# Kernel tuning notes

Hardware: AMD Instinct MI355X
Metric: run time of the kernel (lower is better)

Reference implementation:

```python
import jax, jax.numpy as jnp
import numpy as np

B, S, D_IN, D_MODEL, H = 2, 2048, 1024, 1024, 16
DEPTH = D_MODEL // H


def setup_inputs() -> dict:
    key = jax.random.key(0)
    ks = jax.random.split(key, 12)
    f32 = jnp.float32
    scale = 0.02  # typical init scale for linear weights
    inp = {
        "v": jax.random.normal(ks[0], (B, S, D_IN), f32),
        "k": jax.random.normal(ks[1], (B, S, D_IN), f32),
        "q": jax.random.normal(ks[2], (B, S, D_IN), f32),
        # padding mask: 1 -> masked out, 0 -> keep; broadcastable to (B,H,Sq,Sk)
        "mask": jax.random.randint(ks[3], (B, 1, 1, S), 0, 2).astype(f32),
        # linear params stored as [in, out] so y = x @ W + b (matches torch Linear math)
        "Wq": jax.random.normal(ks[4], (D_IN, D_MODEL), f32) * scale,
        "bq": jnp.zeros((D_MODEL,), f32),
        "Wk": jax.random.normal(ks[5], (D_IN, D_MODEL), f32) * scale,
        "bk": jnp.zeros((D_MODEL,), f32),
        "Wv": jax.random.normal(ks[6], (D_IN, D_MODEL), f32) * scale,
        "bv": jnp.zeros((D_MODEL,), f32),
        "Wo": jax.random.normal(ks[7], (D_MODEL, D_MODEL), f32) * scale,
        "bo": jnp.zeros((D_MODEL,), f32),
    }
    return inp


def _split_heads(x):
    # [B, S, D_MODEL] -> [B, H, S, DEPTH]
    b = x.shape[0]
    return x.reshape(b, -1, H, DEPTH).transpose(0, 2, 1, 3)


def reference(v, k, q, mask, Wq, bq, Wk, bk, Wv, bv, Wo, bo):
    qh = _split_heads(q @ Wq + bq)   # [B,H,Sq,D]
    kh = _split_heads(k @ Wk + bk)   # [B,H,Sk,D]
    vh = _split_heads(v @ Wv + bv)   # [B,H,Sk,D]

    # scaled dot-product attention with additive mask (mask * -1e9)
    inv_sqrt_dk = 1.0 / jnp.sqrt(jnp.float32(DEPTH))
    logits = jnp.einsum('bhqd,bhkd->bhqk', qh, kh) * inv_sqrt_dk
    logits = logits + mask * (-1e9)
    attn = jax.nn.softmax(logits, axis=-1)          # [B,H,Sq,Sk]
    ctx = jnp.einsum('bhqk,bhkd->bhqd', attn, vh)   # [B,H,Sq,D]

    b = q.shape[0]
    concat = ctx.transpose(0, 2, 1, 3).reshape(b, -1, D_MODEL)  # [B,Sq,D_MODEL]
    out = concat @ Wo + bo
    return out, attn
```

## Files before the change

kernel.cpp:

```cpp
#include <hip/hip_runtime.h>
#include <cstdint>
#include <cstddef>

typedef __attribute__((ext_vector_type(4))) float f4;
typedef __attribute__((ext_vector_type(8))) short bf16x8;
typedef __attribute__((ext_vector_type(8))) unsigned short u16x8;
typedef unsigned long long u64;

__device__ __forceinline__ unsigned short f2bf(float x) {
    unsigned u = __float_as_uint(x);
    u += 0x7fffu + ((u >> 16) & 1u);
    return (unsigned short)(u >> 16);
}
__device__ __forceinline__ float bf2f(unsigned short h) {
    return __uint_as_float(((unsigned)h) << 16);
}
__device__ __forceinline__ float fast_exp2(float x) { return __builtin_amdgcn_exp2f(x); }
__device__ __forceinline__ float fast_log2(float x) { return __builtin_amdgcn_logf(x); }
__device__ __forceinline__ void gll16(const void* g, void* l) {
    __builtin_amdgcn_global_load_lds(
        (const __attribute__((address_space(1))) unsigned int*)g,
        (__attribute__((address_space(3))) unsigned int*)l, 16, 0, 0);
}
__device__ __forceinline__ f4 mfma16(bf16x8 a, bf16x8 b, f4 c) {
    return __builtin_amdgcn_mfma_f32_16x16x32_bf16(a, b, c, 0, 0, 0);
}

__global__ __launch_bounds__(256)
void prep_w_kernel(const float* __restrict__ Wq, const float* __restrict__ Wk,
                   const float* __restrict__ Wv, const float* __restrict__ Wo,
                   unsigned short* __restrict__ wt)
{
    const int w = blockIdx.z;
    const float* W = w == 0 ? Wq : (w == 1 ? Wk : (w == 2 ? Wv : Wo));
    unsigned short* hi = wt + (size_t)w * 1048576;

    const int kb = blockIdx.x << 6, nb = blockIdx.y << 6;
    __shared__ float T[64][68];
    const int tid = threadIdx.x;
    {
        const int r = tid >> 2, c0 = (tid & 3) << 4;
        const float* src = W + (size_t)(kb + r) * 1024 + nb + c0;
        *(f4*)&T[r][c0 + 0]  = *(const f4*)(src + 0);
        *(f4*)&T[r][c0 + 4]  = *(const f4*)(src + 4);
        *(f4*)&T[r][c0 + 8]  = *(const f4*)(src + 8);
        *(f4*)&T[r][c0 + 12] = *(const f4*)(src + 12);
    }
    __syncthreads();
    {
        const int n = tid & 63, ks = (tid >> 6) << 4;
        unsigned short vh[16];
        #pragma unroll
        for (int j = 0; j < 16; ++j) vh[j] = f2bf(T[ks + j][n]);
        const size_t dst = (size_t)(nb + n) * 1024 + kb + ks;
        *(u16x8*)(hi + dst)     = *(u16x8*)&vh[0];
        *(u16x8*)(hi + dst + 8) = *(u16x8*)&vh[8];
    }
}

__global__ __launch_bounds__(256)
void prep_a_kernel(const float* __restrict__ q, const float* __restrict__ k,
                   const float* __restrict__ v, unsigned short* __restrict__ a_hi)
{
    const int gid = blockIdx.x * 256 + threadIdx.x;
    const int z = gid >> 18;
    const int rem = gid & 262143;
    const float* src = z == 0 ? q : (z == 1 ? k : v);
    const size_t off = (size_t)rem << 4;
    const float* s = src + off;
    unsigned short* hi = a_hi + ((size_t)z << 22) + off;
    float xs[16];
    *(f4*)&xs[0]  = *(const f4*)(s + 0);
    *(f4*)&xs[4]  = *(const f4*)(s + 4);
    *(f4*)&xs[8]  = *(const f4*)(s + 8);
    *(f4*)&xs[12] = *(const f4*)(s + 12);
    unsigned short hv[16];
    #pragma unroll
    for (int j = 0; j < 16; ++j) hv[j] = f2bf(xs[j]);
    *(u16x8*)(hi + 0) = *(u16x8*)&hv[0];
    *(u16x8*)(hi + 8) = *(u16x8*)&hv[8];
}

__global__ __launch_bounds__(256)
void vtr_kernel(const unsigned short* __restrict__ v_hi, unsigned short* __restrict__ vT)
{
    __shared__ unsigned short T[64][80];
    const int bh = blockIdx.y;
    const int s0 = blockIdx.x << 6;
    const int tid = threadIdx.x;
    const size_t base = (size_t)bh * 131072;
    {
        const int s = tid >> 2, dq = (tid & 3) << 4;
        const unsigned short* src = v_hi + base + (size_t)(s0 + s) * 64 + dq;
        u16x8 a = *(const u16x8*)src;
        u16x8 b = *(const u16x8*)(src + 8);
        *(u16x8*)&T[s][dq]     = a;
        *(u16x8*)&T[s][dq + 8] = b;
    }
    __syncthreads();
    {
        const int d = tid >> 2, sq = (tid & 3) << 4;
        unsigned short o[16];
        #pragma unroll
        for (int j = 0; j < 16; ++j) o[j] = T[sq + j][d];
        unsigned short* dst = vT + base + ((size_t)d << 11) + s0 + sq;
        *(u16x8*)dst       = *(u16x8*)&o[0];
        *(u16x8*)(dst + 8) = *(u16x8*)&o[8];
    }
}

__device__ __forceinline__ void gemm1_core(
    const unsigned short* __restrict__ AH, const unsigned short* __restrict__ WH,
    const float* __restrict__ bias, int bm, int bn, int mode,
    unsigned short* __restrict__ o_hi, float* __restrict__ o_f32, unsigned char* lds)
{
    unsigned char* As = lds;
    unsigned char* Bs = lds + 16384;

    const int tid = threadIdx.x, lane = tid & 63, wave = tid >> 6;
    const int wm = wave >> 1, wn = wave & 1;
    const int cx = lane & 15, lg = lane >> 4;
    const int l3 = lane >> 3, p3 = lane & 7;
    const int m0 = bm << 7, n0 = bn << 7;

    f4 acc[4][4];
    #pragma unroll
    for (int i = 0; i < 4; ++i)
        #pragma unroll
        for (int j = 0; j < 4; ++j) acc[i][j] = (f4){0.f, 0.f, 0.f, 0.f};

    #pragma unroll 1
    for (int k0 = 0; k0 < 1024; k0 += 64) {
        __syncthreads();
        #pragma unroll
        for (int c = 0; c < 4; ++c) {
            const int cb = (c << 2) + wave;
            const int row = (cb << 3) + l3;
            const int lgx = p3 ^ (row & 7);
            gll16(AH + (size_t)(m0 + row) * 1024 + k0 + (lgx << 3),
                  As + (cb << 10) + (lane << 4));
            gll16(WH + (size_t)(n0 + row) * 1024 + k0 + (lgx << 3),
                  Bs + (cb << 10) + (lane << 4));
        }
        __syncthreads();
        #pragma unroll
        for (int ks = 0; ks < 2; ++ks) {
            bf16x8 ah[4], bh[4];
            #pragma unroll
            for (int t = 0; t < 4; ++t) {
                const int r = (wm << 6) + (t << 4) + cx;
                ah[t] = *(const bf16x8*)(As + r * 128 + (((((ks << 2) + lg)) ^ (r & 7)) << 4));
                const int n = (wn << 6) + (t << 4) + cx;
                bh[t] = *(const bf16x8*)(Bs + n * 128 + (((((ks << 2) + lg)) ^ (n & 7)) << 4));
            }
            #pragma unroll
            for (int i = 0; i < 4; ++i)
                #pragma unroll
                for (int j = 0; j < 4; ++j)
                    acc[i][j] = mfma16(ah[i], bh[j], acc[i][j]);
        }
    }

    float bv4[4];
    #pragma unroll
    for (int j = 0; j < 4; ++j) bv4[j] = bias[n0 + (wn << 6) + (j << 4) + cx];

    #pragma unroll
    for (int i = 0; i < 4; ++i)
        #pragma unroll
        for (int j = 0; j < 4; ++j) {
            const int n = n0 + (wn << 6) + (j << 4) + cx;
            const int mb = m0 + (wm << 6) + (i << 4) + (lg << 2);
            if (mode == 2) {
                #pragma unroll
                for (int r = 0; r < 4; ++r)
                    o_f32[(size_t)(mb + r) * 1024 + n] = acc[i][j][r] + bv4[j];
            } else {
                const int b = mb >> 11, hh = n >> 6, d = n & 63;
                #pragma unroll
                for (int r = 0; r < 4; ++r) {
                    const int s = (mb + r) & 2047;
                    o_hi[(((size_t)(b * 16 + hh)) * 2048 + s) * 64 + d] = f2bf(acc[i][j][r] + bv4[j]);
                }
            }
        }
}

__global__ __launch_bounds__(256)
void qkv_gemm_kernel(const unsigned short* __restrict__ a_hi,
                     const unsigned short* __restrict__ wt,
                     const float* __restrict__ bq, const float* __restrict__ bk,
                     const float* __restrict__ bv,
                     unsigned short* __restrict__ q_hi, unsigned short* __restrict__ k_hi,
                     unsigned short* __restrict__ v_hi)
{
    __shared__ __align__(16) unsigned char lds[32768];
    const int f = blockIdx.x;
    const int id2 = (f & 7) * 96 + (f >> 3);
    const int z = id2 >> 8;
    const int rem = id2 & 255;
    const int bn = rem >> 5, bm = rem & 31;
    const unsigned short* AH = a_hi + ((size_t)z << 22);
    const unsigned short* WH = wt + (size_t)z * 1048576;
    const float* bias = z == 0 ? bq : (z == 1 ? bk : bv);
    unsigned short* ohi = z == 0 ? q_hi : (z == 1 ? k_hi : v_hi);
    gemm1_core(AH, WH, bias, bm, bn, 1, ohi, nullptr, lds);
}

__global__ __launch_bounds__(256)
void out_gemm_kernel(const unsigned short* __restrict__ ctx_hi,
                     const unsigned short* __restrict__ wt_o,
                     const float* __restrict__ bo, float* __restrict__ out)
{
    __shared__ __align__(16) unsigned char lds[32768];
    const int f = blockIdx.x;
    const int id2 = (f & 7) * 32 + (f >> 3);
    const int bn = id2 >> 5, bm = id2 & 31;
    gemm1_core(ctx_hi, wt_o, bo, bm, bn, 2, nullptr, out, lds);
}

__global__ __launch_bounds__(256, 4)
void attn_kernel(const unsigned short* __restrict__ q_hi, const unsigned short* __restrict__ k_hi,
                 const unsigned short* __restrict__ vT, const float* __restrict__ mask,
                 float* __restrict__ attn, unsigned short* __restrict__ ctx_hi)
{
    __shared__ __align__(16) unsigned char lds[40960];
    unsigned char* K1 = lds;
    unsigned char* Vs = lds + 16384;
    unsigned char* Ps = lds + 32768;

    const int f = blockIdx.x;
    const int swzf = (f & 7) * 128 + (f >> 3);
    const int bh = swzf >> 5;
    const int q0 = (swzf & 31) << 6;
    const int b = bh >> 4, h = bh & 15;
    const int tid = threadIdx.x, lane = tid & 63, wave = tid >> 6;
    const int cx = lane & 15, lg = lane >> 4;
    const int l3 = lane >> 3, p3 = lane & 7;
    const size_t base = (size_t)bh * 131072;
    const float* mg = mask + (size_t)b * 2048;

    constexpr float C2   = 0.18033688011112042f;
    constexpr float M2   = -1.4426950408889634e9f;
    constexpr float MFIX = 4.0f;

    #pragma unroll
    for (int c = 0; c < 2; ++c) {
        const int cb = (c << 2) + wave;
        const int row = (cb << 3) + l3;
        const int lgx = p3 ^ (row & 7);
        gll16(q_hi + base + (size_t)(q0 + row) * 64 + (lgx << 3),
              Ps + (cb << 10) + (lane << 4));
        gll16(k_hi + base + (size_t)row * 64 + (lgx << 3),
              K1 + (cb << 10) + (lane << 4));
    }
    f4 mrc[4];
    #pragma unroll
    for (int nt = 0; nt < 4; ++nt) mrc[nt] = *(const f4*)(mg + (nt << 4) + (lg << 2));
    asm volatile("s_waitcnt vmcnt(0)" ::: "memory");
    __builtin_amdgcn_s_barrier();

    bf16x8 qb[2];
    {
        const int r = (wave << 4) + cx;
        const int mk = r & 7;
        #pragma unroll
        for (int ks = 0; ks < 2; ++ks)
            qb[ks] = *(const bf16x8*)(Ps + r * 128 + (((((ks << 2) + lg)) ^ mk) << 4));
    }

    float l_loc = 0.f;
    #pragma unroll 1
    for (int t = 0; t < 32; ++t) {
        const int p = t & 1;
        const int k0 = t << 6;
        f4 mrn[4];
        if (t < 31) {
            #pragma unroll
            for (int c = 0; c < 2; ++c) {
                const int cb = (c << 2) + wave;
                const int row = (cb << 3) + l3;
                const int lgx = p3 ^ (row & 7);
                gll16(k_hi + base + (size_t)(k0 + 64 + row) * 64 + (lgx << 3),
                      K1 + ((p ^ 1) << 13) + (cb << 10) + (lane << 4));
            }
            #pragma unroll
            for (int nt = 0; nt < 4; ++nt)
                mrn[nt] = *(const f4*)(mg + k0 + 64 + (nt << 4) + (lg << 2));
        }
        const unsigned char* Kc = K1 + (p << 13);
        __builtin_amdgcn_s_setprio(1);
        f4 sv[4];
        #pragma unroll
        for (int nt = 0; nt < 4; ++nt) {
            const int kr = (nt << 4) + cx;
            const int mk = kr & 7;
            f4 s = (f4){0.f, 0.f, 0.f, 0.f};
            #pragma unroll
            for (int ks = 0; ks < 2; ++ks) {
                const bf16x8 kb = *(const bf16x8*)(Kc + kr * 128 + (((((ks << 2) + lg)) ^ mk) << 4));
                s = mfma16(kb, qb[ks], s);
            }
            sv[nt] = s;
        }
        __builtin_amdgcn_s_setprio(0);
        #pragma unroll
        for (int nt = 0; nt < 4; ++nt)
            #pragma unroll
            for (int r = 0; r < 4; ++r)
                l_loc += fast_exp2(fmaf(sv[nt][r], C2, fmaf(mrc[nt][r], M2, -MFIX)));
        #pragma unroll
        for (int nt = 0; nt < 4; ++nt) mrc[nt] = mrn[nt];
        asm volatile("s_waitcnt vmcnt(0)" ::: "memory");
        __builtin_amdgcn_s_barrier();
    }
    float ssum = l_loc;
    ssum += __shfl_xor(ssum, 16);
    ssum += __shfl_xor(ssum, 32);
    const float cofs = -MFIX - fast_log2(ssum);

    #pragma unroll
    for (int c = 0; c < 2; ++c) {
        const int cb = (c << 2) + wave;
        const int row = (cb << 3) + l3;
        const int lgx = p3 ^ (row & 7);
        gll16(k_hi + base + (size_t)row * 64 + (lgx << 3),
              K1 + (cb << 10) + (lane << 4));
        gll16(vT + base + ((size_t)row << 11) + (lgx << 3),
              Vs + (cb << 10) + (lane << 4));
    }
    #pragma unroll
    for (int nt = 0; nt < 4; ++nt) mrc[nt] = *(const f4*)(mg + (nt << 4) + (lg << 2));
    asm volatile("s_waitcnt vmcnt(0)" ::: "memory");
    __builtin_amdgcn_s_barrier();

    f4 cacc[4];
    #pragma unroll
    for (int nt = 0; nt < 4; ++nt) cacc[nt] = (f4){0.f, 0.f, 0.f, 0.f};

    float* arow = attn + ((size_t)bh * 2048 + q0 + (wave << 4) + cx) * 2048;
    const unsigned psSwz = (unsigned)((cx & 7) << 4);

    #pragma unroll 1
    for (int t = 0; t < 32; ++t) {
        const int p = t & 1;
        const int k0 = t << 6;
        f4 mrn[4];
        if (t < 31) {
            #pragma unroll
            for (int c = 0; c < 2; ++c) {
                const int cb = (c << 2) + wave;
                const int row = (cb << 3) + l3;
                const int lgx = p3 ^ (row & 7);
                gll16(k_hi + base + (size_t)(k0 + 64 + row) * 64 + (lgx << 3),
                      K1 + ((p ^ 1) << 13) + (cb << 10) + (lane << 4));
                gll16(vT + base + ((size_t)row << 11) + k0 + 64 + (lgx << 3),
                      Vs + ((p ^ 1) << 13) + (cb << 10) + (lane << 4));
            }
            #pragma unroll
            for (int nt = 0; nt < 4; ++nt)
                mrn[nt] = *(const f4*)(mg + k0 + 64 + (nt << 4) + (lg << 2));
        }
        const unsigned char* Kc = K1 + (p << 13);
        f4 s[4];
        __builtin_amdgcn_s_setprio(1);
        #pragma unroll
        for (int nt = 0; nt < 4; ++nt) {
            const int kr = (nt << 4) + cx;
            const int mk = kr & 7;
            s[nt] = (f4){0.f, 0.f, 0.f, 0.f};
            #pragma unroll
            for (int ks = 0; ks < 2; ++ks) {
                const bf16x8 kb = *(const bf16x8*)(Kc + kr * 128 + (((((ks << 2) + lg)) ^ mk) << 4));
                s[nt] = mfma16(kb, qb[ks], s[nt]);
            }
        }
        __builtin_amdgcn_s_setprio(0);
        #pragma unroll
        for (int nt = 0; nt < 4; ++nt) {
            f4 pv;
            #pragma unroll
            for (int r = 0; r < 4; ++r)
                pv[r] = fast_exp2(fmaf(s[nt][r], C2, fmaf(mrc[nt][r], M2, cofs)));
            *(f4*)(arow + k0 + (nt << 4) + (lg << 2)) = pv;
            const unsigned w0 = (unsigned)f2bf(pv[0]) | ((unsigned)f2bf(pv[1]) << 16);
            const unsigned w1 = (unsigned)f2bf(pv[2]) | ((unsigned)f2bf(pv[3]) << 16);
            const u64 packed = (u64)w0 | ((u64)w1 << 32);
            *(u64*)(Ps + (((wave << 4) + cx) * 128) +
                    ((unsigned)((nt << 5) + (lg << 3)) ^ psSwz)) = packed;
        }
        #pragma unroll
        for (int nt = 0; nt < 4; ++nt) mrc[nt] = mrn[nt];
        __builtin_amdgcn_s_setprio(1);
        #pragma unroll
        for (int ks = 0; ks < 2; ++ks) {
            const bf16x8 pa = *(const bf16x8*)(Ps + (((wave << 4) + cx) * 128) +
                                ((unsigned)((ks << 6) + (lg << 4)) ^ psSwz));
            #pragma unroll
            for (int nt = 0; nt < 4; ++nt) {
                const int dr = (nt << 4) + cx;
                const bf16x8 vb = *(const bf16x8*)(Vs + (p << 13) + dr * 128 +
                                    (((((ks << 2) + lg)) ^ (dr & 7)) << 4));
                cacc[nt] = mfma16(pa, vb, cacc[nt]);
            }
        }
        __builtin_amdgcn_s_setprio(0);
        asm volatile("s_waitcnt vmcnt(4)" ::: "memory");
        __builtin_amdgcn_s_barrier();
    }

    #pragma unroll
    for (int nt = 0; nt < 4; ++nt)
        #pragma unroll
        for (int r = 0; r < 4; ++r) {
            const int srow = q0 + (wave << 4) + (lg << 2) + r;
            const int d = (h << 6) + (nt << 4) + cx;
            ctx_hi[((size_t)b * 2048 + srow) * 1024 + d] = f2bf(cacc[nt][r]);
        }
}

extern "C" void kernel_launch(void* const* d_in, const int* in_sizes, int n_in,
                              void* d_out, int out_size, void* d_ws, size_t ws_size,
                              hipStream_t stream)
{
    const float* v_in = (const float*)d_in[0];
    const float* k_in = (const float*)d_in[1];
    const float* q_in = (const float*)d_in[2];
    const float* mask = (const float*)d_in[3];
    const float* Wq = (const float*)d_in[4];
    const float* bq = (const float*)d_in[5];
    const float* Wk = (const float*)d_in[6];
    const float* bk = (const float*)d_in[7];
    const float* Wv = (const float*)d_in[8];
    const float* bv = (const float*)d_in[9];
    const float* Wo = (const float*)d_in[10];
    const float* bo = (const float*)d_in[11];

    float* out  = (float*)d_out;
    float* attn = out + (size_t)4194304;

    unsigned char* ws = (unsigned char*)d_ws;
    unsigned short* wt     = (unsigned short*)(ws);
    unsigned short* q_hi   = (unsigned short*)(ws + (size_t)(8)  * 1048576);
    unsigned short* k_hi   = (unsigned short*)(ws + (size_t)(16) * 1048576);
    unsigned short* v_hi   = (unsigned short*)(ws + (size_t)(24) * 1048576);
    unsigned short* ctx_hi = (unsigned short*)(ws + (size_t)(32) * 1048576);
    unsigned short* vT     = (unsigned short*)(ws + (size_t)(40) * 1048576);

    unsigned short* a_hi   = (unsigned short*)(attn + (size_t)60 * 1048576);

    prep_w_kernel<<<dim3(16, 16, 4), 256, 0, stream>>>(Wq, Wk, Wv, Wo, wt);
    prep_a_kernel<<<3072, 256, 0, stream>>>(q_in, k_in, v_in, a_hi);
    qkv_gemm_kernel<<<768, 256, 0, stream>>>(a_hi, wt, bq, bk, bv, q_hi, k_hi, v_hi);
    vtr_kernel<<<dim3(32, 32), 256, 0, stream>>>(v_hi, vT);
    attn_kernel<<<1024, 256, 0, stream>>>(q_hi, k_hi, vT, mask, attn, ctx_hi);
    out_gemm_kernel<<<256, 256, 0, stream>>>(ctx_hi, wt + (size_t)3 * 1048576, bo, out);
}
```

Before: 293.2 us.

## Load K/V/Q fragments directly from global memory, dropping LDS staging and barriers

Removes the double-buffered LDS staging of K, V and Q via global_load_lds, along with the per-iteration barriers and waitcnts. Each wave now reads its MFMA operand fragments straight from global memory (relying on L1/L2 since the four waves share K/V tiles), and LDS shrinks to the P scratch only. This removes synchronisation overhead and raises possible occupancy, but gives up the explicit prefetch overlap and issues redundant global reads across waves.

```diff
diff --git a/kernel.cpp b/kernel.cpp
--- a/kernel.cpp
+++ b/kernel.cpp
@@ -224,10 +224,7 @@
                  const unsigned short* __restrict__ vT, const float* __restrict__ mask,
                  float* __restrict__ attn, unsigned short* __restrict__ ctx_hi)
 {
-    __shared__ __align__(16) unsigned char lds[40960];
-    unsigned char* K1 = lds;
-    unsigned char* Vs = lds + 16384;
-    unsigned char* Ps = lds + 32768;
+    __shared__ __align__(16) unsigned char Ps[8192];
 
     const int f = blockIdx.x;
     const int swzf = (f & 7) * 128 + (f >> 3);
@@ -236,7 +233,6 @@
     const int b = bh >> 4, h = bh & 15;
     const int tid = threadIdx.x, lane = tid & 63, wave = tid >> 6;
     const int cx = lane & 15, lg = lane >> 4;
-    const int l3 = lane >> 3, p3 = lane & 7;
     const size_t base = (size_t)bh * 131072;
     const float* mg = mask + (size_t)b * 2048;
 
@@ -244,96 +240,37 @@
     constexpr float M2   = -1.4426950408889634e9f;
     constexpr float MFIX = 4.0f;
 
-    #pragma unroll
-    for (int c = 0; c < 2; ++c) {
-        const int cb = (c << 2) + wave;
-        const int row = (cb << 3) + l3;
-        const int lgx = p3 ^ (row & 7);
-        gll16(q_hi + base + (size_t)(q0 + row) * 64 + (lgx << 3),
-              Ps + (cb << 10) + (lane << 4));
-        gll16(k_hi + base + (size_t)row * 64 + (lgx << 3),
-              K1 + (cb << 10) + (lane << 4));
-    }
-    f4 mrc[4];
-    #pragma unroll
-    for (int nt = 0; nt < 4; ++nt) mrc[nt] = *(const f4*)(mg + (nt << 4) + (lg << 2));
-    asm volatile("s_waitcnt vmcnt(0)" ::: "memory");
-    __builtin_amdgcn_s_barrier();
-
     bf16x8 qb[2];
-    {
-        const int r = (wave << 4) + cx;
-        const int mk = r & 7;
-        #pragma unroll
-        for (int ks = 0; ks < 2; ++ks)
-            qb[ks] = *(const bf16x8*)(Ps + r * 128 + (((((ks << 2) + lg)) ^ mk) << 4));
-    }
+    #pragma unroll
+    for (int ks = 0; ks < 2; ++ks)
+        qb[ks] = *(const bf16x8*)(q_hi + base + (size_t)(q0 + (wave << 4) + cx) * 64
+                                  + (((ks << 2) + lg) << 3));
 
     float l_loc = 0.f;
     #pragma unroll 1
     for (int t = 0; t < 32; ++t) {
-        const int p = t & 1;
         const int k0 = t << 6;
-        f4 mrn[4];
-        if (t < 31) {
-            #pragma unroll
-            for (int c = 0; c < 2; ++c) {
-                const int cb = (c << 2) + wave;
-                const int row = (cb << 3) + l3;
-                const int lgx = p3 ^ (row & 7);
-                gll16(k_hi + base + (size_t)(k0 + 64 + row) * 64 + (lgx << 3),
-                      K1 + ((p ^ 1) << 13) + (cb << 10) + (lane << 4));
-            }
-            #pragma unroll
-            for (int nt = 0; nt < 4; ++nt)
-                mrn[nt] = *(const f4*)(mg + k0 + 64 + (nt << 4) + (lg << 2));
-        }
-        const unsigned char* Kc = K1 + (p << 13);
-        __builtin_amdgcn_s_setprio(1);
-        f4 sv[4];
         #pragma unroll
         for (int nt = 0; nt < 4; ++nt) {
-            const int kr = (nt << 4) + cx;
-            const int mk = kr & 7;
             f4 s = (f4){0.f, 0.f, 0.f, 0.f};
             #pragma unroll
             for (int ks = 0; ks < 2; ++ks) {
-                const bf16x8 kb = *(const bf16x8*)(Kc + kr * 128 + (((((ks << 2) + lg)) ^ mk) << 4));
+                const bf16x8 kb = *(const bf16x8*)(k_hi + base
+                    + (size_t)(k0 + (nt << 4) + cx) * 64 + (((ks << 2) + lg) << 3));
                 s = mfma16(kb, qb[ks], s);
             }
-            sv[nt] = s;
-        }
-        __builtin_amdgcn_s_setprio(0);
-        #pragma unroll
-        for (int nt = 0; nt < 4; ++nt)
-            #pragma unroll
-            for (int r = 0; r < 4; ++r)
-                l_loc += fast_exp2(fmaf(sv[nt][r], C2, fmaf(mrc[nt][r], M2, -MFIX)));
-        #pragma unroll
-        for (int nt = 0; nt < 4; ++nt) mrc[nt] = mrn[nt];
-        asm volatile("s_waitcnt vmcnt(0)" ::: "memory");
-        __builtin_amdgcn_s_barrier();
+            const f4 ml = *(const f4*)(mg + k0 + (nt << 4) + (lg << 2));
+            l_loc += fast_exp2(fmaf(s[0], C2, fmaf(ml[0], M2, -MFIX)))
+                   + fast_exp2(fmaf(s[1], C2, fmaf(ml[1], M2, -MFIX)))
+                   + fast_exp2(fmaf(s[2], C2, fmaf(ml[2], M2, -MFIX)))
+                   + fast_exp2(fmaf(s[3], C2, fmaf(ml[3], M2, -MFIX)));
+        }
     }
     float ssum = l_loc;
     ssum += __shfl_xor(ssum, 16);
     ssum += __shfl_xor(ssum, 32);
     const float cofs = -MFIX - fast_log2(ssum);
 
-    #pragma unroll
-    for (int c = 0; c < 2; ++c) {
-        const int cb = (c << 2) + wave;
-        const int row = (cb << 3) + l3;
-        const int lgx = p3 ^ (row & 7);
-        gll16(k_hi + base + (size_t)row * 64 + (lgx << 3),
-              K1 + (cb << 10) + (lane << 4));
-        gll16(vT + base + ((size_t)row << 11) + (lgx << 3),
-              Vs + (cb << 10) + (lane << 4));
-    }
-    #pragma unroll
-    for (int nt = 0; nt < 4; ++nt) mrc[nt] = *(const f4*)(mg + (nt << 4) + (lg << 2));
-    asm volatile("s_waitcnt vmcnt(0)" ::: "memory");
-    __builtin_amdgcn_s_barrier();
-
     f4 cacc[4];
     #pragma unroll
     for (int nt = 0; nt < 4; ++nt) cacc[nt] = (f4){0.f, 0.f, 0.f, 0.f};
@@ -343,45 +280,25 @@
 
     #pragma unroll 1
     for (int t = 0; t < 32; ++t) {
-        const int p = t & 1;
         const int k0 = t << 6;
-        f4 mrn[4];
-        if (t < 31) {
-            #pragma unroll
-            for (int c = 0; c < 2; ++c) {
-                const int cb = (c << 2) + wave;
-                const int row = (cb << 3) + l3;
-                const int lgx = p3 ^ (row & 7);
-                gll16(k_hi + base + (size_t)(k0 + 64 + row) * 64 + (lgx << 3),
-                      K1 + ((p ^ 1) << 13) + (cb << 10) + (lane << 4));
-                gll16(vT + base + ((size_t)row << 11) + k0 + 64 + (lgx << 3),
-                      Vs + ((p ^ 1) << 13) + (cb << 10) + (lane << 4));
-            }
-            #pragma unroll
-            for (int nt = 0; nt < 4; ++nt)
-                mrn[nt] = *(const f4*)(mg + k0 + 64 + (nt << 4) + (lg << 2));
-        }
-        const unsigned char* Kc = K1 + (p << 13);
         f4 s[4];
-        __builtin_amdgcn_s_setprio(1);
         #pragma unroll
         for (int nt = 0; nt < 4; ++nt) {
-            const int kr = (nt << 4) + cx;
-            const int mk = kr & 7;
             s[nt] = (f4){0.f, 0.f, 0.f, 0.f};
             #pragma unroll
             for (int ks = 0; ks < 2; ++ks) {
-                const bf16x8 kb = *(const bf16x8*)(Kc + kr * 128 + (((((ks << 2) + lg)) ^ mk) << 4));
+                const bf16x8 kb = *(const bf16x8*)(k_hi + base
+                    + (size_t)(k0 + (nt << 4) + cx) * 64 + (((ks << 2) + lg) << 3));
                 s[nt] = mfma16(kb, qb[ks], s[nt]);
             }
         }
-        __builtin_amdgcn_s_setprio(0);
         #pragma unroll
         for (int nt = 0; nt < 4; ++nt) {
+            const f4 ml = *(const f4*)(mg + k0 + (nt << 4) + (lg << 2));
             f4 pv;
             #pragma unroll
             for (int r = 0; r < 4; ++r)
-                pv[r] = fast_exp2(fmaf(s[nt][r], C2, fmaf(mrc[nt][r], M2, cofs)));
+                pv[r] = fast_exp2(fmaf(s[nt][r], C2, fmaf(ml[r], M2, cofs)));
             *(f4*)(arow + k0 + (nt << 4) + (lg << 2)) = pv;
             const unsigned w0 = (unsigned)f2bf(pv[0]) | ((unsigned)f2bf(pv[1]) << 16);
             const unsigned w1 = (unsigned)f2bf(pv[2]) | ((unsigned)f2bf(pv[3]) << 16);
@@ -390,23 +307,16 @@
                     ((unsigned)((nt << 5) + (lg << 3)) ^ psSwz)) = packed;
         }
         #pragma unroll
-        for (int nt = 0; nt < 4; ++nt) mrc[nt] = mrn[nt];
-        __builtin_amdgcn_s_setprio(1);
-        #pragma unroll
         for (int ks = 0; ks < 2; ++ks) {
             const bf16x8 pa = *(const bf16x8*)(Ps + (((wave << 4) + cx) * 128) +
                                 ((unsigned)((ks << 6) + (lg << 4)) ^ psSwz));
             #pragma unroll
             for (int nt = 0; nt < 4; ++nt) {
-                const int dr = (nt << 4) + cx;
-                const bf16x8 vb = *(const bf16x8*)(Vs + (p << 13) + dr * 128 +
-                                    (((((ks << 2) + lg)) ^ (dr & 7)) << 4));
+                const bf16x8 vb = *(const bf16x8*)(vT + base
+                    + ((size_t)((nt << 4) + cx) << 11) + k0 + (((ks << 2) + lg) << 3));
                 cacc[nt] = mfma16(pa, vb, cacc[nt]);
             }
         }
-        __builtin_amdgcn_s_setprio(0);
-        asm volatile("s_waitcnt vmcnt(4)" ::: "memory");
-        __builtin_amdgcn_s_barrier();
     }
 
     #pragma unroll
```

Result: slower. 536.4 us (+82.9%).

## Double attention query tile to 128 rows per block for K/V reuse

Applied to the files above, without the earlier changes.

The attention kernel now processes 128 query rows per block (two 16-row subtiles per wave) instead of 64, halving the grid and sharing each loaded K/V tile and each K fragment across twice as many MFMAs. It also switches bf16 packing to the hardware v_cvt_pk_bf16_f32 instruction and adjusts waitcnt depths and sched barriers. In exchange it raises LDS use to 48KB, lowers the occupancy hint to 3 blocks per CU, and increases register pressure.

```diff
diff --git a/kernel.cpp b/kernel.cpp
--- a/kernel.cpp
+++ b/kernel.cpp
@@ -14,6 +14,11 @@
 }
 __device__ __forceinline__ float bf2f(unsigned short h) {
     return __uint_as_float(((unsigned)h) << 16);
+}
+__device__ __forceinline__ unsigned cvtpk_bf16(float lo, float hi) {
+    unsigned r;
+    asm("v_cvt_pk_bf16_f32 %0, %1, %2" : "=v"(r) : "v"(lo), "v"(hi));
+    return r;
 }
 __device__ __forceinline__ float fast_exp2(float x) { return __builtin_amdgcn_exp2f(x); }
 __device__ __forceinline__ float fast_log2(float x) { return __builtin_amdgcn_logf(x); }
@@ -219,20 +224,20 @@
     gemm1_core(ctx_hi, wt_o, bo, bm, bn, 2, nullptr, out, lds);
 }
 
-__global__ __launch_bounds__(256, 4)
+__global__ __launch_bounds__(256, 3)
 void attn_kernel(const unsigned short* __restrict__ q_hi, const unsigned short* __restrict__ k_hi,
                  const unsigned short* __restrict__ vT, const float* __restrict__ mask,
                  float* __restrict__ attn, unsigned short* __restrict__ ctx_hi)
 {
-    __shared__ __align__(16) unsigned char lds[40960];
+    __shared__ __align__(16) unsigned char lds[49152];
     unsigned char* K1 = lds;
     unsigned char* Vs = lds + 16384;
     unsigned char* Ps = lds + 32768;
 
     const int f = blockIdx.x;
-    const int swzf = (f & 7) * 128 + (f >> 3);
-    const int bh = swzf >> 5;
-    const int q0 = (swzf & 31) << 6;
+    const int swzf = (f & 7) * 64 + (f >> 3);
+    const int bh = swzf >> 4;
+    const int q0 = (swzf & 15) << 7;
     const int b = bh >> 4, h = bh & 15;
     const int tid = threadIdx.x, lane = tid & 63, wave = tid >> 6;
     const int cx = lane & 15, lg = lane >> 4;
@@ -245,12 +250,18 @@
     constexpr float MFIX = 4.0f;
 
     #pragma unroll
-    for (int c = 0; c < 2; ++c) {
+    for (int c = 0; c < 4; ++c) {
         const int cb = (c << 2) + wave;
         const int row = (cb << 3) + l3;
         const int lgx = p3 ^ (row & 7);
         gll16(q_hi + base + (size_t)(q0 + row) * 64 + (lgx << 3),
               Ps + (cb << 10) + (lane << 4));
+    }
+    #pragma unroll
+    for (int c = 0; c < 2; ++c) {
+        const int cb = (c << 2) + wave;
+        const int row = (cb << 3) + l3;
+        const int lgx = p3 ^ (row & 7);
         gll16(k_hi + base + (size_t)row * 64 + (lgx << 3),
               K1 + (cb << 10) + (lane << 4));
     }
@@ -260,16 +271,17 @@
     asm volatile("s_waitcnt vmcnt(0)" ::: "memory");
     __builtin_amdgcn_s_barrier();
 
-    bf16x8 qb[2];
-    {
-        const int r = (wave << 4) + cx;
+    bf16x8 qb[2][2];
+    #pragma unroll
+    for (int qs = 0; qs < 2; ++qs) {
+        const int r = (wave << 5) + (qs << 4) + cx;
         const int mk = r & 7;
         #pragma unroll
         for (int ks = 0; ks < 2; ++ks)
-            qb[ks] = *(const bf16x8*)(Ps + r * 128 + (((((ks << 2) + lg)) ^ mk) << 4));
-    }
-
-    float l_loc = 0.f;
+            qb[qs][ks] = *(const bf16x8*)(Ps + r * 128 + (((((ks << 2) + lg)) ^ mk) << 4));
+    }
+
+    float l4[2][2] = {{0.f, 0.f}, {0.f, 0.f}};
     #pragma unroll 1
     for (int t = 0; t < 32; ++t) {
         const int p = t & 1;
@@ -284,40 +296,47 @@
                 gll16(k_hi + base + (size_t)(k0 + 64 + row) * 64 + (lgx << 3),
                       K1 + ((p ^ 1) << 13) + (cb << 10) + (lane << 4));
             }
+            __builtin_amdgcn_sched_barrier(0);
             #pragma unroll
             for (int nt = 0; nt < 4; ++nt)
                 mrn[nt] = *(const f4*)(mg + k0 + 64 + (nt << 4) + (lg << 2));
         }
         const unsigned char* Kc = K1 + (p << 13);
-        __builtin_amdgcn_s_setprio(1);
-        f4 sv[4];
         #pragma unroll
         for (int nt = 0; nt < 4; ++nt) {
             const int kr = (nt << 4) + cx;
             const int mk = kr & 7;
-            f4 s = (f4){0.f, 0.f, 0.f, 0.f};
-            #pragma unroll
-            for (int ks = 0; ks < 2; ++ks) {
-                const bf16x8 kb = *(const bf16x8*)(Kc + kr * 128 + (((((ks << 2) + lg)) ^ mk) << 4));
-                s = mfma16(kb, qb[ks], s);
-            }
-            sv[nt] = s;
-        }
-        __builtin_amdgcn_s_setprio(0);
-        #pragma unroll
-        for (int nt = 0; nt < 4; ++nt)
-            #pragma unroll
-            for (int r = 0; r < 4; ++r)
-                l_loc += fast_exp2(fmaf(sv[nt][r], C2, fmaf(mrc[nt][r], M2, -MFIX)));
+            const bf16x8 kb0 = *(const bf16x8*)(Kc + kr * 128 + ((lg ^ mk) << 4));
+            const bf16x8 kb1 = *(const bf16x8*)(Kc + kr * 128 + (((4 + lg) ^ mk) << 4));
+            __builtin_amdgcn_s_setprio(1);
+            f4 s0 = mfma16(kb0, qb[0][0], (f4){0.f, 0.f, 0.f, 0.f});
+            s0 = mfma16(kb1, qb[0][1], s0);
+            f4 s1 = mfma16(kb0, qb[1][0], (f4){0.f, 0.f, 0.f, 0.f});
+            s1 = mfma16(kb1, qb[1][1], s1);
+            __builtin_amdgcn_s_setprio(0);
+            const f4 mv = mrc[nt];
+            l4[0][nt & 1] += fast_exp2(fmaf(s0[0], C2, fmaf(mv[0], M2, -MFIX)))
+                           + fast_exp2(fmaf(s0[1], C2, fmaf(mv[1], M2, -MFIX)))
+                           + fast_exp2(fmaf(s0[2], C2, fmaf(mv[2], M2, -MFIX)))
+                           + fast_exp2(fmaf(s0[3], C2, fmaf(mv[3], M2, -MFIX)));
+            l4[1][nt & 1] += fast_exp2(fmaf(s1[0], C2, fmaf(mv[0], M2, -MFIX)))
+                           + fast_exp2(fmaf(s1[1], C2, fmaf(mv[1], M2, -MFIX)))
+                           + fast_exp2(fmaf(s1[2], C2, fmaf(mv[2], M2, -MFIX)))
+                           + fast_exp2(fmaf(s1[3], C2, fmaf(mv[3], M2, -MFIX)));
+        }
         #pragma unroll
         for (int nt = 0; nt < 4; ++nt) mrc[nt] = mrn[nt];
-        asm volatile("s_waitcnt vmcnt(0)" ::: "memory");
+        asm volatile("s_waitcnt vmcnt(4)" ::: "memory");
         __builtin_amdgcn_s_barrier();
     }
-    float ssum = l_loc;
-    ssum += __shfl_xor(ssum, 16);
-    ssum += __shfl_xor(ssum, 32);
-    const float cofs = -MFIX - fast_log2(ssum);
+    float cofs[2];
+    #pragma unroll
+    for (int qs = 0; qs < 2; ++qs) {
+        float ss = l4[qs][0] + l4[qs][1];
+        ss += __shfl_xor(ss, 16);
+        ss += __shfl_xor(ss, 32);
+        cofs[qs] = -MFIX - fast_log2(ss);
+    }
 
     #pragma unroll
     for (int c = 0; c < 2; ++c) {
@@ -334,11 +353,14 @@
     asm volatile("s_waitcnt vmcnt(0)" ::: "memory");
     __builtin_amdgcn_s_barrier();
 
-    f4 cacc[4];
-    #pragma unroll
-    for (int nt = 0; nt < 4; ++nt) cacc[nt] = (f4){0.f, 0.f, 0.f, 0.f};
-
-    float* arow = attn + ((size_t)bh * 2048 + q0 + (wave << 4) + cx) * 2048;
+    f4 cacc[2][4];
+    #pragma unroll
+    for (int qs = 0; qs < 2; ++qs)
+        #pragma unroll
+        for (int nt = 0; nt < 4; ++nt) cacc[qs][nt] = (f4){0.f, 0.f, 0.f, 0.f};
+
+    float* arow0 = attn + ((size_t)bh * 2048 + q0 + (wave << 5) + cx) * 2048;
+    float* arow1 = arow0 + (size_t)16 * 2048;
     const unsigned psSwz = (unsigned)((cx & 7) << 4);
 
     #pragma unroll 1
@@ -357,66 +379,77 @@
                 gll16(vT + base + ((size_t)row << 11) + k0 + 64 + (lgx << 3),
                       Vs + ((p ^ 1) << 13) + (cb << 10) + (lane << 4));
             }
+            __builtin_amdgcn_sched_barrier(0);
             #pragma unroll
             for (int nt = 0; nt < 4; ++nt)
                 mrn[nt] = *(const f4*)(mg + k0 + 64 + (nt << 4) + (lg << 2));
         }
         const unsigned char* Kc = K1 + (p << 13);
-        f4 s[4];
-        __builtin_amdgcn_s_setprio(1);
+        f4 s[2][4];
         #pragma unroll
         for (int nt = 0; nt < 4; ++nt) {
             const int kr = (nt << 4) + cx;
             const int mk = kr & 7;
-            s[nt] = (f4){0.f, 0.f, 0.f, 0.f};
-            #pragma unroll
-            for (int ks = 0; ks < 2; ++ks) {
-                const bf16x8 kb = *(const bf16x8*)(Kc + kr * 128 + (((((ks << 2) + lg)) ^ mk) << 4));
-                s[nt] = mfma16(kb, qb[ks], s[nt]);
-            }
-        }
-        __builtin_amdgcn_s_setprio(0);
-        #pragma unroll
-        for (int nt = 0; nt < 4; ++nt) {
-            f4 pv;
-            #pragma unroll
-            for (int r = 0; r < 4; ++r)
-                pv[r] = fast_exp2(fmaf(s[nt][r], C2, fmaf(mrc[nt][r], M2, cofs)));
-            *(f4*)(arow + k0 + (nt << 4) + (lg << 2)) = pv;
-            const unsigned w0 = (unsigned)f2bf(pv[0]) | ((unsigned)f2bf(pv[1]) << 16);
-            const unsigned w1 = (unsigned)f2bf(pv[2]) | ((unsigned)f2bf(pv[3]) << 16);
-            const u64 packed = (u64)w0 | ((u64)w1 << 32);
-            *(u64*)(Ps + (((wave << 4) + cx) * 128) +
-                    ((unsigned)((nt << 5) + (lg << 3)) ^ psSwz)) = packed;
+            const bf16x8 kb0 = *(const bf16x8*)(Kc + kr * 128 + ((lg ^ mk) << 4));
+            const bf16x8 kb1 = *(const bf16x8*)(Kc + kr * 128 + (((4 + lg) ^ mk) << 4));
+            __builtin_amdgcn_s_setprio(1);
+            s[0][nt] = mfma16(kb0, qb[0][0], (f4){0.f, 0.f, 0.f, 0.f});
+            s[0][nt] = mfma16(kb1, qb[0][1], s[0][nt]);
+            s[1][nt] = mfma16(kb0, qb[1][0], (f4){0.f, 0.f, 0.f, 0.f});
+            s[1][nt] = mfma16(kb1, qb[1][1], s[1][nt]);
+            __builtin_amdgcn_s_setprio(0);
+        }
+        #pragma unroll
+        for (int qs = 0; qs < 2; ++qs) {
+            float* arow = qs ? arow1 : arow0;
+            const unsigned psRow = (unsigned)(((wave << 5) + (qs << 4) + cx) * 128);
+            #pragma unroll
+            for (int nt = 0; nt < 4; ++nt) {
+                f4 pv;
+                #pragma unroll
+                for (int r = 0; r < 4; ++r)
+                    pv[r] = fast_exp2(fmaf(s[qs][nt][r], C2, fmaf(mrc[nt][r], M2, cofs[qs])));
+                *(f4*)(arow + k0 + (nt << 4) + (lg << 2)) = pv;
+                const unsigned w0 = cvtpk_bf16(pv[0], pv[1]);
+                const unsigned w1 = cvtpk_bf16(pv[2], pv[3]);
+                const u64 packed = (u64)w0 | ((u64)w1 << 32);
+                *(u64*)(Ps + psRow + ((unsigned)((nt << 5) + (lg << 3)) ^ psSwz)) = packed;
+            }
         }
         #pragma unroll
         for (int nt = 0; nt < 4; ++nt) mrc[nt] = mrn[nt];
-        __builtin_amdgcn_s_setprio(1);
         #pragma unroll
         for (int ks = 0; ks < 2; ++ks) {
-            const bf16x8 pa = *(const bf16x8*)(Ps + (((wave << 4) + cx) * 128) +
-                                ((unsigned)((ks << 6) + (lg << 4)) ^ psSwz));
+            bf16x8 pa[2];
+            #pragma unroll
+            for (int qs = 0; qs < 2; ++qs)
+                pa[qs] = *(const bf16x8*)(Ps + (((wave << 5) + (qs << 4) + cx) * 128) +
+                                          ((unsigned)((ks << 6) + (lg << 4)) ^ psSwz));
             #pragma unroll
             for (int nt = 0; nt < 4; ++nt) {
                 const int dr = (nt << 4) + cx;
                 const bf16x8 vb = *(const bf16x8*)(Vs + (p << 13) + dr * 128 +
                                     (((((ks << 2) + lg)) ^ (dr & 7)) << 4));
-                cacc[nt] = mfma16(pa, vb, cacc[nt]);
-            }
-        }
-        __builtin_amdgcn_s_setprio(0);
-        asm volatile("s_waitcnt vmcnt(4)" ::: "memory");
+                __builtin_amdgcn_s_setprio(1);
+                cacc[0][nt] = mfma16(pa[0], vb, cacc[0][nt]);
+                cacc[1][nt] = mfma16(pa[1], vb, cacc[1][nt]);
+                __builtin_amdgcn_s_setprio(0);
+            }
+        }
+        asm volatile("s_waitcnt vmcnt(8)" ::: "memory");
         __builtin_amdgcn_s_barrier();
     }
 
     #pragma unroll
-    for (int nt = 0; nt < 4; ++nt)
-        #pragma unroll
-        for (int r = 0; r < 4; ++r) {
-            const int srow = q0 + (wave << 4) + (lg << 2) + r;
-            const int d = (h << 6) + (nt << 4) + cx;
-            ctx_hi[((size_t)b * 2048 + srow) * 1024 + d] = f2bf(cacc[nt][r]);
-        }
+    for (int qs = 0; qs < 2; ++qs)
+        #pragma unroll
+        for (int nt = 0; nt < 4; ++nt)
+            #pragma unroll
+            for (int r = 0; r < 4; ++r) {
+                const int srow = q0 + (wave << 5) + (qs << 4) + (lg << 2) + r;
+                const int d = (h << 6) + (nt << 4) + cx;
+                ctx_hi[((size_t)b * 2048 + srow) * 1024 + d] = f2bf(cacc[qs][nt][r]);
+            }
 }
 
 extern "C" void kernel_launch(void* const* d_in, const int* in_sizes, int n_in,
@@ -453,6 +486,6 @@
     prep_a_kernel<<<3072, 256, 0, stream>>>(q_in, k_in, v_in, a_hi);
     qkv_gemm_kernel<<<768, 256, 0, stream>>>(a_hi, wt, bq, bk, bv, q_hi, k_hi, v_hi);
     vtr_kernel<<<dim3(32, 32), 256, 0, stream>>>(v_hi, vT);
-    attn_kernel<<<1024, 256, 0, stream>>>(q_hi, k_hi, vT, mask, attn, ctx_hi);
+    attn_kernel<<<512, 256, 0, stream>>>(q_hi, k_hi, vT, mask, attn, ctx_hi);
     out_gemm_kernel<<<256, 256, 0, stream>>>(ctx_hi, wt + (size_t)3 * 1048576, bo, out);
 }
```

Measured after the change: 286.7 us. -2.2%, faster.

## Register-prefetch K in attention stats pass and use packed bf16 convert

Applied to the files above, without the earlier changes.

The first (softmax-denominator) pass of the attention kernel no longer stages Q and K through LDS with barriers. Each wave loads its Q and K MFMA fragments straight from global memory into registers, double-buffered with ping-pong arrays, and the exp-sum accumulates into four partial sums. In the second pass, the manual float-to-bf16 rounding is replaced by the hardware v_cvt_pk_bf16_f32 instruction, and a scheduling barrier is added after the K/V LDS loads. Occupancy hint drops from 4 to 3 blocks per CU to make room for the extra registers, which risks less latency hiding.

```diff
diff --git a/kernel.cpp b/kernel.cpp
--- a/kernel.cpp
+++ b/kernel.cpp
@@ -14,6 +14,11 @@
 }
 __device__ __forceinline__ float bf2f(unsigned short h) {
     return __uint_as_float(((unsigned)h) << 16);
+}
+__device__ __forceinline__ unsigned cvtpk_bf16(float lo, float hi) {
+    unsigned r;
+    asm("v_cvt_pk_bf16_f32 %0, %1, %2" : "=v"(r) : "v"(lo), "v"(hi));
+    return r;
 }
 __device__ __forceinline__ float fast_exp2(float x) { return __builtin_amdgcn_exp2f(x); }
 __device__ __forceinline__ float fast_log2(float x) { return __builtin_amdgcn_logf(x); }
@@ -219,7 +224,7 @@
     gemm1_core(ctx_hi, wt_o, bo, bm, bn, 2, nullptr, out, lds);
 }
 
-__global__ __launch_bounds__(256, 4)
+__global__ __launch_bounds__(256, 3)
 void attn_kernel(const unsigned short* __restrict__ q_hi, const unsigned short* __restrict__ k_hi,
                  const unsigned short* __restrict__ vT, const float* __restrict__ mask,
                  float* __restrict__ attn, unsigned short* __restrict__ ctx_hi)
@@ -244,77 +249,63 @@
     constexpr float M2   = -1.4426950408889634e9f;
     constexpr float MFIX = 4.0f;
 
-    #pragma unroll
-    for (int c = 0; c < 2; ++c) {
-        const int cb = (c << 2) + wave;
-        const int row = (cb << 3) + l3;
-        const int lgx = p3 ^ (row & 7);
-        gll16(q_hi + base + (size_t)(q0 + row) * 64 + (lgx << 3),
-              Ps + (cb << 10) + (lane << 4));
-        gll16(k_hi + base + (size_t)row * 64 + (lgx << 3),
-              K1 + (cb << 10) + (lane << 4));
-    }
-    f4 mrc[4];
-    #pragma unroll
-    for (int nt = 0; nt < 4; ++nt) mrc[nt] = *(const f4*)(mg + (nt << 4) + (lg << 2));
-    asm volatile("s_waitcnt vmcnt(0)" ::: "memory");
-    __builtin_amdgcn_s_barrier();
-
     bf16x8 qb[2];
-    {
-        const int r = (wave << 4) + cx;
-        const int mk = r & 7;
+    #pragma unroll
+    for (int ks = 0; ks < 2; ++ks)
+        qb[ks] = *(const bf16x8*)(q_hi + base + (size_t)(q0 + (wave << 4) + cx) * 64
+                                  + (((ks << 2) + lg) << 3));
+
+    float l4[4] = {0.f, 0.f, 0.f, 0.f};
+
+    const unsigned short* kfrag_base = k_hi + base + (size_t)cx * 64 + (((0 << 2) + lg) << 3);
+
+    bf16x8 kA[4][2], kB[4][2];
+    f4 mA[4], mB[4];
+
+    #pragma unroll
+    for (int nt = 0; nt < 4; ++nt) {
+        const size_t r = (size_t)((nt << 4) + cx) * 64;
         #pragma unroll
         for (int ks = 0; ks < 2; ++ks)
-            qb[ks] = *(const bf16x8*)(Ps + r * 128 + (((((ks << 2) + lg)) ^ mk) << 4));
-    }
-
-    float l_loc = 0.f;
+            kA[nt][ks] = *(const bf16x8*)(k_hi + base + r + (((ks << 2) + lg) << 3));
+        mA[nt] = *(const f4*)(mg + (nt << 4) + (lg << 2));
+    }
+
+    auto p1_body = [&](bf16x8 (&kc)[4][2], bf16x8 (&kn)[4][2],
+                       f4 (&mc)[4], f4 (&mn)[4], int t) {
+        const int k0 = t << 6;
+        if (t < 31) {
+            #pragma unroll
+            for (int nt = 0; nt < 4; ++nt) {
+                const size_t r = (size_t)(k0 + 64 + (nt << 4) + cx) * 64;
+                #pragma unroll
+                for (int ks = 0; ks < 2; ++ks)
+                    kn[nt][ks] = *(const bf16x8*)(k_hi + base + r + (((ks << 2) + lg) << 3));
+                mn[nt] = *(const f4*)(mg + k0 + 64 + (nt << 4) + (lg << 2));
+            }
+        }
+        f4 s[4];
+        #pragma unroll
+        for (int nt = 0; nt < 4; ++nt) {
+            s[nt] = mfma16(kc[nt][0], qb[0], (f4){0.f, 0.f, 0.f, 0.f});
+            s[nt] = mfma16(kc[nt][1], qb[1], s[nt]);
+        }
+        #pragma unroll
+        for (int nt = 0; nt < 4; ++nt) {
+            l4[nt] += fast_exp2(fmaf(s[nt][0], C2, fmaf(mc[nt][0], M2, -MFIX)))
+                    + fast_exp2(fmaf(s[nt][1], C2, fmaf(mc[nt][1], M2, -MFIX)))
+                    + fast_exp2(fmaf(s[nt][2], C2, fmaf(mc[nt][2], M2, -MFIX)))
+                    + fast_exp2(fmaf(s[nt][3], C2, fmaf(mc[nt][3], M2, -MFIX)));
+        }
+    };
+
     #pragma unroll 1
-    for (int t = 0; t < 32; ++t) {
-        const int p = t & 1;
-        const int k0 = t << 6;
-        f4 mrn[4];
-        if (t < 31) {
-            #pragma unroll
-            for (int c = 0; c < 2; ++c) {
-                const int cb = (c << 2) + wave;
-                const int row = (cb << 3) + l3;
-                const int lgx = p3 ^ (row & 7);
-                gll16(k_hi + base + (size_t)(k0 + 64 + row) * 64 + (lgx << 3),
-                      K1 + ((p ^ 1) << 13) + (cb << 10) + (lane << 4));
-            }
-            #pragma unroll
-            for (int nt = 0; nt < 4; ++nt)
-                mrn[nt] = *(const f4*)(mg + k0 + 64 + (nt << 4) + (lg << 2));
-        }
-        const unsigned char* Kc = K1 + (p << 13);
-        __builtin_amdgcn_s_setprio(1);
-        f4 sv[4];
-        #pragma unroll
-        for (int nt = 0; nt < 4; ++nt) {
-            const int kr = (nt << 4) + cx;
-            const int mk = kr & 7;
-            f4 s = (f4){0.f, 0.f, 0.f, 0.f};
-            #pragma unroll
-            for (int ks = 0; ks < 2; ++ks) {
-                const bf16x8 kb = *(const bf16x8*)(Kc + kr * 128 + (((((ks << 2) + lg)) ^ mk) << 4));
-                s = mfma16(kb, qb[ks], s);
-            }
-            sv[nt] = s;
-        }
-        __builtin_amdgcn_s_setprio(0);
-        #pragma unroll
-        for (int nt = 0; nt < 4; ++nt)
-            #pragma unroll
-            for (int r = 0; r < 4; ++r)
-                l_loc += fast_exp2(fmaf(sv[nt][r], C2, fmaf(mrc[nt][r], M2, -MFIX)));
-        #pragma unroll
-        for (int nt = 0; nt < 4; ++nt) mrc[nt] = mrn[nt];
-        asm volatile("s_waitcnt vmcnt(0)" ::: "memory");
-        __builtin_amdgcn_s_barrier();
-    }
-    float ssum = l_loc;
+    for (int t = 0; t < 32; t += 2) {
+        p1_body(kA, kB, mA, mB, t);
+        p1_body(kB, kA, mB, mA, t + 1);
+    }
+
+    float ssum = (l4[0] + l4[1]) + (l4[2] + l4[3]);
     ssum += __shfl_xor(ssum, 16);
     ssum += __shfl_xor(ssum, 32);
     const float cofs = -MFIX - fast_log2(ssum);
@@ -329,6 +320,7 @@
         gll16(vT + base + ((size_t)row << 11) + (lgx << 3),
               Vs + (cb << 10) + (lane << 4));
     }
+    f4 mrc[4];
     #pragma unroll
     for (int nt = 0; nt < 4; ++nt) mrc[nt] = *(const f4*)(mg + (nt << 4) + (lg << 2));
     asm volatile("s_waitcnt vmcnt(0)" ::: "memory");
@@ -357,6 +349,7 @@
                 gll16(vT + base + ((size_t)row << 11) + k0 + 64 + (lgx << 3),
                       Vs + ((p ^ 1) << 13) + (cb << 10) + (lane << 4));
             }
+            __builtin_amdgcn_sched_barrier(0);
             #pragma unroll
             for (int nt = 0; nt < 4; ++nt)
                 mrn[nt] = *(const f4*)(mg + k0 + 64 + (nt << 4) + (lg << 2));
@@ -383,8 +376,8 @@
             for (int r = 0; r < 4; ++r)
                 pv[r] = fast_exp2(fmaf(s[nt][r], C2, fmaf(mrc[nt][r], M2, cofs)));
             *(f4*)(arow + k0 + (nt << 4) + (lg << 2)) = pv;
-            const unsigned w0 = (unsigned)f2bf(pv[0]) | ((unsigned)f2bf(pv[1]) << 16);
-            const unsigned w1 = (unsigned)f2bf(pv[2]) | ((unsigned)f2bf(pv[3]) << 16);
+            const unsigned w0 = cvtpk_bf16(pv[0], pv[1]);
+            const unsigned w1 = cvtpk_bf16(pv[2], pv[3]);
             const u64 packed = (u64)w0 | ((u64)w1 << 32);
             *(u64*)(Ps + (((wave << 4) + cx) * 128) +
                     ((unsigned)((nt << 5) + (lg << 3)) ^ psSwz)) = packed;
```

New measurement: 373.2 us. 27.3% more time.
